# Kernel tuning notes

Measured on AMD Instinct MI355X. Metric: run time of the kernel, lower is better.

The kernel has to match this reference:

```python
import jax, jax.numpy as jnp
import numpy as np

WS = (7, 7)          # window size
N = WS[0] * WS[1]    # 49 tokens per window
C = 128              # dim
H = 4                # num heads
D = C // H           # head dim = 32
B = 8192             # batch * num_windows
NW = 1024            # windows per image
SCALE = D ** -0.5


def _relative_position_index():
    coords_h = np.arange(WS[0])
    coords_w = np.arange(WS[1])
    coords = np.stack(np.meshgrid(coords_h, coords_w, indexing='ij'))  # [2,Wh,Ww]
    flat = coords.reshape(2, -1)                                        # [2,N]
    rel = flat[:, :, None] - flat[:, None, :]                           # [2,N,N]
    rel = rel.transpose(1, 2, 0).astype(np.int64)                       # [N,N,2]
    rel[:, :, 0] += WS[0] - 1
    rel[:, :, 1] += WS[1] - 1
    rel[:, :, 0] *= 2 * WS[1] - 1
    return rel.sum(-1)                                                  # [N,N]


def setup_inputs() -> dict:
    key = jax.random.key(0)
    ks = jax.random.split(key, 8)
    s = 0.02
    return {
        'x': jax.random.normal(ks[0], (B, N, C), jnp.float32),
        'y': jax.random.normal(ks[1], (B, N, C), jnp.float32),
        'mask': jnp.zeros((NW, N, N), jnp.float32),
        'Wq': jax.random.normal(ks[2], (C, C), jnp.float32) * s,
        'bq': jnp.zeros((C,), jnp.float32),
        'Wkv': jax.random.normal(ks[3], (C, 2 * C), jnp.float32) * s,
        'bkv': jnp.zeros((2 * C,), jnp.float32),
        'bias_table': jax.random.normal(ks[4], ((2 * WS[0] - 1) * (2 * WS[1] - 1), H), jnp.float32) * s,
        'Wp': jax.random.normal(ks[5], (C, C), jnp.float32) * s,
        'bp': jnp.zeros((C,), jnp.float32),
        'rel_idx': jnp.asarray(_relative_position_index(), jnp.int32),
    }


def reference(x, y, mask, Wq, bq, Wkv, bkv, bias_table, Wp, bp, rel_idx):
    b = x.shape[0]
    # q/kv projections
    q = (x @ Wq + bq).reshape(b, N, H, D).transpose(0, 2, 1, 3) * SCALE   # [B,H,N,D]
    kv = (y @ Wkv + bkv).reshape(b, N, 2, H, D).transpose(2, 0, 3, 1, 4)  # [2,B,H,N,D]
    k, v = kv[0], kv[1]
    attn = jnp.einsum('bhnd,bhmd->bhnm', q, k)                            # [B,H,N,N]
    # relative position bias gather
    bias = bias_table[rel_idx.reshape(-1)].reshape(N, N, H).transpose(2, 0, 1)  # [H,N,N]
    attn = attn + bias[None]
    # mask add per window
    nW = mask.shape[0]
    attn = attn.reshape(b // nW, nW, H, N, N) + mask[None, :, None]
    attn = attn.reshape(b, H, N, N)
    attn = jax.nn.softmax(attn, axis=-1)
    out = jnp.einsum('bhnm,bhmd->bhnd', attn, v)                          # [B,H,N,D]
    out = out.transpose(0, 2, 1, 3).reshape(b, N, C)
    return out @ Wp + bp
```

## Files before the change

kernel.cpp:

```cpp
#include <hip/hip_runtime.h>
#include <cstddef>


#define MFMA16 __builtin_amdgcn_mfma_f32_16x16x32_bf16

typedef float f32x4 __attribute__((ext_vector_type(4)));
typedef __bf16 bf16x8 __attribute__((ext_vector_type(8)));
typedef __bf16 bf16x4 __attribute__((ext_vector_type(4)));

constexpr int NTOK = 49;
constexpr int CDIM = 128;
constexpr int NWIN = 1024;
constexpr int NB = 8192;
constexpr float SCALE_F = 0.17677669529663687f;

__device__ __forceinline__ int sw128(int row, int col) {
  return (row << 8) + ((((col >> 3) ^ row) & 15) << 4) + ((col & 7) << 1);
}
__device__ __forceinline__ int sw64(int row, int col) {
  return (row << 7) + ((((col >> 3) ^ (row >> 1)) & 7) << 4) + ((col & 7) << 1);
}
__device__ __forceinline__ int swp(int m, int nl) {
  return (m << 6) + ((((nl >> 3) ^ (m >> 1)) & 3) << 4) + ((nl & 7) << 1);
}

__global__ void prepack_kernel(const float* __restrict__ Wq, const float* __restrict__ Wkv,
                               const float* __restrict__ Wp, const float* __restrict__ bias_table,
                               const int* __restrict__ rel_idx,
                               unsigned short* __restrict__ wFrag, float* __restrict__ biasM) {
  int t = blockIdx.x * 256 + threadIdx.x;
  if (t < 8192) {
    const int mat = t >> 11;
    const int g = t & 2047;
    const int frag = g >> 6, lane = g & 63;
    const int nt = frag >> 2, ks = frag & 3;
    const int li = lane & 15, q4 = lane >> 4;
    const int n = nt * 16 + li;
    bf16x8 tmp;
#pragma unroll
    for (int j = 0; j < 8; ++j) {
      const int k = ks * 32 + q4 * 8 + j;
      float v;
      if (mat == 0) v = Wq[k * 128 + n];
      else if (mat == 1) v = Wkv[k * 256 + n];
      else if (mat == 2) v = Wkv[k * 256 + 128 + n];
      else v = Wp[k * 128 + n];
      tmp[j] = (__bf16)v;
    }
    *(bf16x8*)(wFrag + (size_t)t * 8) = tmp;
  } else {
    const int tb = t - 8192;
    if (tb < 4 * 49 * 64) {
      const int h = tb / 3136;
      const int rem = tb - h * 3136;
      const int m = rem >> 6, n = rem & 63;
      float v = 0.f;
      if (n < NTOK) v = bias_table[rel_idx[m * 49 + n] * 4 + h];
      biasM[tb] = v;
    }
  }
}

__global__ void maskM_kernel(const float* __restrict__ mask, float* __restrict__ maskM) {
  __shared__ float sm[2401];
  const int w = blockIdx.x;
  for (int i = threadIdx.x; i < 2401; i += 256) sm[i] = mask[(size_t)w * 2401 + i];
  __syncthreads();
  for (int i = threadIdx.x; i < 3136; i += 256) {
    const int m = i >> 6, n = i & 63;
    maskM[(size_t)w * 3136 + i] = (n < NTOK) ? sm[m * 49 + n] : -1e30f;
  }
}

template <bool PADMASK>
__global__ __launch_bounds__(256, 4) void attn_kernel(
    const float* __restrict__ x, const float* __restrict__ y, const float* __restrict__ maskp,
    const float* __restrict__ bq, const float* __restrict__ bkv, const float* __restrict__ bp,
    const unsigned short* __restrict__ wFrag, const float* __restrict__ biasM,
    float* __restrict__ out) {
  __shared__ __align__(16) unsigned char lds[32768];
  const int tid = threadIdx.x;
  const int w = tid >> 6;
  const int lane = tid & 63;
  const int li = lane & 15;
  const int q4 = lane >> 4;
  const int b = blockIdx.x;
  const int mh = w >> 1;
  const int nh = w & 1;

  bf16x8 ax[2][4], ay[2][4];
#pragma unroll
  for (int t = 0; t < 2; ++t) {
    const int mrow = mh * 32 + t * 16 + li;
    const bool mv = mrow < NTOK;
    const float* xr = x + ((size_t)b * NTOK + (mv ? mrow : 0)) * CDIM;
    const float* yr = y + ((size_t)b * NTOK + (mv ? mrow : 0)) * CDIM;
#pragma unroll
    for (int ks = 0; ks < 4; ++ks) {
      const int c0 = ks * 32 + q4 * 8;
      float4 a0 = *(const float4*)(xr + c0);
      float4 a1 = *(const float4*)(xr + c0 + 4);
      float4 b0 = *(const float4*)(yr + c0);
      float4 b1 = *(const float4*)(yr + c0 + 4);
      if (!mv) {
        a0.x = a0.y = a0.z = a0.w = 0.f; a1.x = a1.y = a1.z = a1.w = 0.f;
        b0.x = b0.y = b0.z = b0.w = 0.f; b1.x = b1.y = b1.z = b1.w = 0.f;
      }
      bf16x8 ta, tb;
      ta[0] = (__bf16)a0.x; ta[1] = (__bf16)a0.y; ta[2] = (__bf16)a0.z; ta[3] = (__bf16)a0.w;
      ta[4] = (__bf16)a1.x; ta[5] = (__bf16)a1.y; ta[6] = (__bf16)a1.z; ta[7] = (__bf16)a1.w;
      tb[0] = (__bf16)b0.x; tb[1] = (__bf16)b0.y; tb[2] = (__bf16)b0.z; tb[3] = (__bf16)b0.w;
      tb[4] = (__bf16)b1.x; tb[5] = (__bf16)b1.y; tb[6] = (__bf16)b1.z; tb[7] = (__bf16)b1.w;
      ax[t][ks] = ta;
      ay[t][ks] = tb;
    }
  }

  const unsigned short* wq = wFrag + 0 * 16384 + nh * 8192;
  const unsigned short* wk = wFrag + 1 * 16384 + nh * 8192;
  const unsigned short* wv = wFrag + 2 * 16384 + nh * 8192;
  const unsigned short* wp = wFrag + 3 * 16384 + nh * 8192;

  auto ldw = [&](const unsigned short* base, int ntl, bf16x8* dst) {
#pragma unroll
    for (int ks = 0; ks < 4; ++ks)
      dst[ks] = *(const bf16x8*)(base + (ntl * 4 + ks) * 512 + lane * 8);
  };

  bf16x8 wfb[2][4];
  bf16x4 vpk[2][4];
  ldw(wq, 0, wfb[0]);
#pragma unroll
  for (int s = 0; s < 12; ++s) {
    if (s < 11) {
      const int nn = s + 1;
      ldw(nn < 4 ? wq : (nn < 8 ? wk : wv), nn & 3, wfb[nn & 1]);
    }
    const int mat = s >> 2, ntl = s & 3;
    const bf16x8* wf = wfb[s & 1];
    if (mat < 2) {
      const int ch0 = nh * 64 + ntl * 16 + q4 * 4;
      const float4 b4 = *(const float4*)((mat == 0 ? bq : bkv) + ch0);
      const int ldsoff = (mat == 0) ? 0 : 16384;
#pragma unroll
      for (int t = 0; t < 2; ++t) {
        const bf16x8* af = (mat == 0) ? &ax[t][0] : &ay[t][0];
        f32x4 acc = {0.f, 0.f, 0.f, 0.f};
#pragma unroll
        for (int ks = 0; ks < 4; ++ks) acc = MFMA16(wf[ks], af[ks], acc, 0, 0, 0);
        const int tok = mh * 32 + t * 16 + li;
        bf16x4 pv;
        pv[0] = (__bf16)(acc[0] + b4.x); pv[1] = (__bf16)(acc[1] + b4.y);
        pv[2] = (__bf16)(acc[2] + b4.z); pv[3] = (__bf16)(acc[3] + b4.w);
        *(bf16x4*)(lds + ldsoff + sw128(tok, ch0)) = pv;
      }
    } else {
      const int nV = nh * 64 + ntl * 16 + li;
      const float bvv = bkv[128 + nV];
#pragma unroll
      for (int t = 0; t < 2; ++t) {
        f32x4 acc = {0.f, 0.f, 0.f, 0.f};
#pragma unroll
        for (int ks = 0; ks < 4; ++ks) acc = MFMA16(ay[t][ks], wf[ks], acc, 0, 0, 0);
        bf16x4 vv4;
        vv4[0] = (__bf16)(acc[0] + bvv); vv4[1] = (__bf16)(acc[1] + bvv);
        vv4[2] = (__bf16)(acc[2] + bvv); vv4[3] = (__bf16)(acc[3] + bvv);
        vpk[t][ntl] = vv4;
      }
    }
  }
  __syncthreads();

  const int h = w;
  unsigned char* const pbase = lds + w * 4096;
  bf16x8 aqf[4], bkf[4];
#pragma unroll
  for (int mt = 0; mt < 4; ++mt)
    aqf[mt] = *(const bf16x8*)(lds + sw128(mt * 16 + li, h * 32 + q4 * 8));
#pragma unroll
  for (int nt = 0; nt < 4; ++nt)
    bkf[nt] = *(const bf16x8*)(lds + 16384 + sw128(nt * 16 + li, h * 32 + q4 * 8));

  const float* __restrict__ biasw = biasM + h * 3136;
  const float* __restrict__ maskw =
      PADMASK ? maskp + (size_t)(b & (NWIN - 1)) * 3136 : maskp + (size_t)(b & (NWIN - 1)) * 2401;

  auto ldbm = [&](int mt, f32x4* dst) {
    const int m = mt * 16 + li;
    const int mm = (m < NTOK ? m : 0);
#pragma unroll
    for (int nt = 0; nt < 4; ++nt) {
      const int nc = nt * 16 + q4 * 4;
      const f32x4 bv = *(const f32x4*)(biasw + mm * 64 + nc);
      f32x4 mv;
      if (PADMASK) {
        mv = *(const f32x4*)(maskw + mm * 64 + nc);
      } else {
#pragma unroll
        for (int r = 0; r < 4; ++r) {
          const int n = nc + r;
          mv[r] = (n < NTOK) ? maskw[mm * 49 + n] : -1e30f;
        }
      }
      dst[nt] = bv + mv;
    }
  };

  f32x4 bmv[2][4];
  ldbm(0, bmv[0]);
  __syncthreads();

#pragma unroll
  for (int ntl = 0; ntl < 4; ++ntl) {
    const int nV = nh * 64 + ntl * 16 + li;
#pragma unroll
    for (int t = 0; t < 2; ++t)
      *(bf16x4*)(lds + 16384 + sw64(nV, mh * 32 + t * 16 + q4 * 4)) = vpk[t][ntl];
  }

  float inv4[4];
  bf16x4 pHi[4][2];
  const f32x4 zz = {0.f, 0.f, 0.f, 0.f};
#pragma unroll
  for (int mt = 0; mt < 4; ++mt) {
    if (mt < 3) ldbm(mt + 1, bmv[(mt + 1) & 1]);
    f32x4 s4[4];
#pragma unroll
    for (int nt = 0; nt < 4; ++nt) s4[nt] = MFMA16(bkf[nt], aqf[mt], zz, 0, 0, 0);
    const f32x4* bm = bmv[mt & 1];
    float vv[4][4];
    float mx = -3.0e38f;
#pragma unroll
    for (int nt = 0; nt < 4; ++nt)
#pragma unroll
      for (int r = 0; r < 4; ++r) {
        const float tv = fmaf(SCALE_F, s4[nt][r], bm[nt][r]);
        vv[nt][r] = tv;
        mx = fmaxf(mx, tv);
      }
    mx = fmaxf(mx, __shfl_xor(mx, 16));
    mx = fmaxf(mx, __shfl_xor(mx, 32));
    float sm = 0.f;
#pragma unroll
    for (int nt = 0; nt < 4; ++nt)
#pragma unroll
      for (int r = 0; r < 4; ++r) {
        const float e = __expf(vv[nt][r] - mx);
        vv[nt][r] = e;
        sm += e;
      }
    sm += __shfl_xor(sm, 16);
    sm += __shfl_xor(sm, 32);
    inv4[mt] = __builtin_amdgcn_rcpf(sm);
    bf16x4 p0, p1;
    p0[0] = (__bf16)vv[0][0]; p0[1] = (__bf16)vv[0][1];
    p0[2] = (__bf16)vv[0][2]; p0[3] = (__bf16)vv[0][3];
    p1[0] = (__bf16)vv[1][0]; p1[1] = (__bf16)vv[1][1];
    p1[2] = (__bf16)vv[1][2]; p1[3] = (__bf16)vv[1][3];
    *(bf16x4*)(pbase + swp(mt * 16 + li, q4 * 4)) = p0;
    *(bf16x4*)(pbase + swp(mt * 16 + li, 16 + q4 * 4)) = p1;
    bf16x4 h0, h1;
    h0[0] = (__bf16)vv[2][0]; h0[1] = (__bf16)vv[2][1];
    h0[2] = (__bf16)vv[2][2]; h0[3] = (__bf16)vv[2][3];
    h1[0] = (__bf16)vv[3][0]; h1[1] = (__bf16)vv[3][1];
    h1[2] = (__bf16)vv[3][2]; h1[3] = (__bf16)vv[3][3];
    pHi[mt][0] = h0;
    pHi[mt][1] = h1;
  }
  __syncthreads();

  bf16x8 bv2[2][2];
#pragma unroll
  for (int cht = 0; cht < 2; ++cht)
#pragma unroll
    for (int ksn = 0; ksn < 2; ++ksn)
      bv2[cht][ksn] =
          *(const bf16x8*)(lds + 16384 + sw64(h * 32 + cht * 16 + li, ksn * 32 + q4 * 8));
  f32x4 o[2][4];
  {
    bf16x8 ap[4];
#pragma unroll
    for (int mt = 0; mt < 4; ++mt)
      ap[mt] = *(const bf16x8*)(pbase + swp(mt * 16 + li, q4 * 8));
#pragma unroll
    for (int cht = 0; cht < 2; ++cht)
#pragma unroll
      for (int mt = 0; mt < 4; ++mt) o[cht][mt] = MFMA16(bv2[cht][0], ap[mt], zz, 0, 0, 0);
#pragma unroll
    for (int mt = 0; mt < 4; ++mt) {
      *(bf16x4*)(pbase + swp(mt * 16 + li, q4 * 4)) = pHi[mt][0];
      *(bf16x4*)(pbase + swp(mt * 16 + li, 16 + q4 * 4)) = pHi[mt][1];
    }
#pragma unroll
    for (int mt = 0; mt < 4; ++mt)
      ap[mt] = *(const bf16x8*)(pbase + swp(mt * 16 + li, q4 * 8));
#pragma unroll
    for (int cht = 0; cht < 2; ++cht)
#pragma unroll
      for (int mt = 0; mt < 4; ++mt)
        o[cht][mt] = MFMA16(bv2[cht][1], ap[mt], o[cht][mt], 0, 0, 0);
  }
  __syncthreads();

#pragma unroll
  for (int cht = 0; cht < 2; ++cht)
#pragma unroll
    for (int mt = 0; mt < 4; ++mt) {
      bf16x4 zv;
      zv[0] = (__bf16)(o[cht][mt][0] * inv4[mt]);
      zv[1] = (__bf16)(o[cht][mt][1] * inv4[mt]);
      zv[2] = (__bf16)(o[cht][mt][2] * inv4[mt]);
      zv[3] = (__bf16)(o[cht][mt][3] * inv4[mt]);
      *(bf16x4*)(lds + sw128(mt * 16 + li, h * 32 + cht * 16 + q4 * 4)) = zv;
    }
  ldw(wp, 0, wfb[0]);
  __syncthreads();

  bf16x8 az[2][4];
#pragma unroll
  for (int t = 0; t < 2; ++t)
#pragma unroll
    for (int ks = 0; ks < 4; ++ks)
      az[t][ks] = *(const bf16x8*)(lds + sw128(mh * 32 + t * 16 + li, ks * 32 + q4 * 8));
#pragma unroll
  for (int ntl = 0; ntl < 4; ++ntl) {
    if (ntl < 3) ldw(wp, ntl + 1, wfb[(ntl + 1) & 1]);
    const bf16x8* wf = wfb[ntl & 1];
    const int ch0 = nh * 64 + ntl * 16 + q4 * 4;
    const float4 b4 = *(const float4*)(bp + ch0);
#pragma unroll
    for (int t = 0; t < 2; ++t) {
      f32x4 acc = {0.f, 0.f, 0.f, 0.f};
#pragma unroll
      for (int ks = 0; ks < 4; ++ks) acc = MFMA16(wf[ks], az[t][ks], acc, 0, 0, 0);
      const int tok = mh * 32 + t * 16 + li;
      if (tok < NTOK) {
        float4 st;
        st.x = acc[0] + b4.x; st.y = acc[1] + b4.y;
        st.z = acc[2] + b4.z; st.w = acc[3] + b4.w;
        *(float4*)(out + ((size_t)b * NTOK + tok) * CDIM + ch0) = st;
      }
    }
  }
}

extern "C" void kernel_launch(void* const* d_in, const int* in_sizes, int n_in, void* d_out,
                              int out_size, void* d_ws, size_t ws_size, hipStream_t stream) {
  const float* x = (const float*)d_in[0];
  const float* y = (const float*)d_in[1];
  const float* mask = (const float*)d_in[2];
  const float* Wq = (const float*)d_in[3];
  const float* bq = (const float*)d_in[4];
  const float* Wkv = (const float*)d_in[5];
  const float* bkv = (const float*)d_in[6];
  const float* bt = (const float*)d_in[7];
  const float* Wp = (const float*)d_in[8];
  const float* bp = (const float*)d_in[9];
  const int* rel = (const int*)d_in[10];
  float* out = (float*)d_out;

  unsigned short* wFrag = (unsigned short*)d_ws;
  float* biasM = (float*)((char*)d_ws + 131072);
  float* maskM = (float*)((char*)d_ws + 181248);
  const size_t needM = 181248 + (size_t)NWIN * 3136 * sizeof(float);

  prepack_kernel<<<96, 256, 0, stream>>>(Wq, Wkv, Wp, bt, rel, wFrag, biasM);
  if (ws_size >= needM) {
    maskM_kernel<<<NWIN, 256, 0, stream>>>(mask, maskM);
    attn_kernel<true><<<NB, 256, 0, stream>>>(x, y, maskM, bq, bkv, bp, wFrag, biasM, out);
  } else {
    attn_kernel<false><<<NB, 256, 0, stream>>>(x, y, mask, bq, bkv, bp, wFrag, biasM, out);
  }
}
```

Measured before the change: 703.0 us.

## Presum bias+mask per window-head, defer V projection, triple-buffer weights, add setprio

Replaces the padded mask table with a per-window, per-head table that already holds relative-position bias plus mask, so the attention loop does one load instead of two loads and an add. This table is four times larger, which adds more preprocessing writes and more L2/HBM traffic. The V projection now runs after the first barrier, overlapping it with the Q/K fragment reads, and weight fragments go through a three-deep register buffer. MFMA blocks are wrapped in s_setprio, launch bounds drop from 4 to 3 blocks per SM, and masking of padded x/y rows is removed, which may raise register use and lower occupancy.

Result: faster. 638.4 us (-9.2%).

```diff
diff --git a/kernel.cpp b/kernel.cpp
--- a/kernel.cpp
+++ b/kernel.cpp
@@ -61,19 +61,33 @@
   }
 }
 
-__global__ void maskM_kernel(const float* __restrict__ mask, float* __restrict__ maskM) {
-  __shared__ float sm[2401];
+__global__ void bmsum_kernel(const float* __restrict__ mask, const float* __restrict__ bias_table,
+                             const int* __restrict__ rel_idx, float* __restrict__ bmSum) {
+  __shared__ float smk[2401];
+  __shared__ int ri[2401];
+  __shared__ float bt[169 * 4];
   const int w = blockIdx.x;
-  for (int i = threadIdx.x; i < 2401; i += 256) sm[i] = mask[(size_t)w * 2401 + i];
+  for (int i = threadIdx.x; i < 2401; i += 256) {
+    smk[i] = mask[(size_t)w * 2401 + i];
+    ri[i] = rel_idx[i];
+  }
+  for (int i = threadIdx.x; i < 676; i += 256) bt[i] = bias_table[i];
   __syncthreads();
   for (int i = threadIdx.x; i < 3136; i += 256) {
     const int m = i >> 6, n = i & 63;
-    maskM[(size_t)w * 3136 + i] = (n < NTOK) ? sm[m * 49 + n] : -1e30f;
-  }
-}
-
-template <bool PADMASK>
-__global__ __launch_bounds__(256, 4) void attn_kernel(
+    const bool valid = (n < NTOK);
+    const int mi = m * 49 + (valid ? n : 0);
+    const float base = smk[mi];
+    const int r = ri[mi];
+#pragma unroll
+    for (int h = 0; h < 4; ++h) {
+      bmSum[((size_t)w * 4 + h) * 3136 + i] = valid ? (bt[r * 4 + h] + base) : -1e30f;
+    }
+  }
+}
+
+template <bool PRESUM>
+__global__ __launch_bounds__(256, 3) void attn_kernel(
     const float* __restrict__ x, const float* __restrict__ y, const float* __restrict__ maskp,
     const float* __restrict__ bq, const float* __restrict__ bkv, const float* __restrict__ bp,
     const unsigned short* __restrict__ wFrag, const float* __restrict__ biasM,
@@ -92,20 +106,16 @@
 #pragma unroll
   for (int t = 0; t < 2; ++t) {
     const int mrow = mh * 32 + t * 16 + li;
-    const bool mv = mrow < NTOK;
-    const float* xr = x + ((size_t)b * NTOK + (mv ? mrow : 0)) * CDIM;
-    const float* yr = y + ((size_t)b * NTOK + (mv ? mrow : 0)) * CDIM;
+    const int mm = mrow < NTOK ? mrow : 0;
+    const float* xr = x + ((size_t)b * NTOK + mm) * CDIM;
+    const float* yr = y + ((size_t)b * NTOK + mm) * CDIM;
 #pragma unroll
     for (int ks = 0; ks < 4; ++ks) {
       const int c0 = ks * 32 + q4 * 8;
-      float4 a0 = *(const float4*)(xr + c0);
-      float4 a1 = *(const float4*)(xr + c0 + 4);
-      float4 b0 = *(const float4*)(yr + c0);
-      float4 b1 = *(const float4*)(yr + c0 + 4);
-      if (!mv) {
-        a0.x = a0.y = a0.z = a0.w = 0.f; a1.x = a1.y = a1.z = a1.w = 0.f;
-        b0.x = b0.y = b0.z = b0.w = 0.f; b1.x = b1.y = b1.z = b1.w = 0.f;
-      }
+      const float4 a0 = *(const float4*)(xr + c0);
+      const float4 a1 = *(const float4*)(xr + c0 + 4);
+      const float4 b0 = *(const float4*)(yr + c0);
+      const float4 b1 = *(const float4*)(yr + c0 + 4);
       bf16x8 ta, tb;
       ta[0] = (__bf16)a0.x; ta[1] = (__bf16)a0.y; ta[2] = (__bf16)a0.z; ta[3] = (__bf16)a0.w;
       ta[4] = (__bf16)a1.x; ta[5] = (__bf16)a1.y; ta[6] = (__bf16)a1.z; ta[7] = (__bf16)a1.w;
@@ -120,6 +130,7 @@
   const unsigned short* wk = wFrag + 1 * 16384 + nh * 8192;
   const unsigned short* wv = wFrag + 2 * 16384 + nh * 8192;
   const unsigned short* wp = wFrag + 3 * 16384 + nh * 8192;
+  const unsigned short* mats01[2] = {wq, wk};
 
   auto ldw = [&](const unsigned short* base, int ntl, bf16x8* dst) {
 #pragma unroll
@@ -127,48 +138,35 @@
       dst[ks] = *(const bf16x8*)(base + (ntl * 4 + ks) * 512 + lane * 8);
   };
 
-  bf16x8 wfb[2][4];
-  bf16x4 vpk[2][4];
+  bf16x8 wfb[3][4];
   ldw(wq, 0, wfb[0]);
-#pragma unroll
-  for (int s = 0; s < 12; ++s) {
-    if (s < 11) {
-      const int nn = s + 1;
-      ldw(nn < 4 ? wq : (nn < 8 ? wk : wv), nn & 3, wfb[nn & 1]);
+  ldw(wq, 1, wfb[1]);
+#pragma unroll
+  for (int s = 0; s < 8; ++s) {
+    if (s < 6) {
+      const int nn = s + 2;
+      ldw(mats01[nn >> 2], nn & 3, wfb[nn % 3]);
     }
     const int mat = s >> 2, ntl = s & 3;
-    const bf16x8* wf = wfb[s & 1];
-    if (mat < 2) {
-      const int ch0 = nh * 64 + ntl * 16 + q4 * 4;
-      const float4 b4 = *(const float4*)((mat == 0 ? bq : bkv) + ch0);
-      const int ldsoff = (mat == 0) ? 0 : 16384;
-#pragma unroll
-      for (int t = 0; t < 2; ++t) {
-        const bf16x8* af = (mat == 0) ? &ax[t][0] : &ay[t][0];
-        f32x4 acc = {0.f, 0.f, 0.f, 0.f};
-#pragma unroll
-        for (int ks = 0; ks < 4; ++ks) acc = MFMA16(wf[ks], af[ks], acc, 0, 0, 0);
-        const int tok = mh * 32 + t * 16 + li;
-        bf16x4 pv;
-        pv[0] = (__bf16)(acc[0] + b4.x); pv[1] = (__bf16)(acc[1] + b4.y);
-        pv[2] = (__bf16)(acc[2] + b4.z); pv[3] = (__bf16)(acc[3] + b4.w);
-        *(bf16x4*)(lds + ldsoff + sw128(tok, ch0)) = pv;
-      }
-    } else {
-      const int nV = nh * 64 + ntl * 16 + li;
-      const float bvv = bkv[128 + nV];
-#pragma unroll
-      for (int t = 0; t < 2; ++t) {
-        f32x4 acc = {0.f, 0.f, 0.f, 0.f};
-#pragma unroll
-        for (int ks = 0; ks < 4; ++ks) acc = MFMA16(ay[t][ks], wf[ks], acc, 0, 0, 0);
-        bf16x4 vv4;
-        vv4[0] = (__bf16)(acc[0] + bvv); vv4[1] = (__bf16)(acc[1] + bvv);
-        vv4[2] = (__bf16)(acc[2] + bvv); vv4[3] = (__bf16)(acc[3] + bvv);
-        vpk[t][ntl] = vv4;
-      }
-    }
-  }
+    const bf16x8* wf = wfb[s % 3];
+    const int ch0 = nh * 64 + ntl * 16 + q4 * 4;
+    const float4 b4 = *(const float4*)((mat == 0 ? bq : bkv) + ch0);
+    const int ldsoff = (mat == 0) ? 0 : 16384;
+#pragma unroll
+    for (int t = 0; t < 2; ++t) {
+      const bf16x8* af = (mat == 0) ? &ax[t][0] : &ay[t][0];
+      f32x4 acc = {0.f, 0.f, 0.f, 0.f};
+#pragma unroll
+      for (int ks = 0; ks < 4; ++ks) acc = MFMA16(wf[ks], af[ks], acc, 0, 0, 0);
+      const int tok = mh * 32 + t * 16 + li;
+      bf16x4 pv;
+      pv[0] = (__bf16)(acc[0] + b4.x); pv[1] = (__bf16)(acc[1] + b4.y);
+      pv[2] = (__bf16)(acc[2] + b4.z); pv[3] = (__bf16)(acc[3] + b4.w);
+      *(bf16x4*)(lds + ldsoff + sw128(tok, ch0)) = pv;
+    }
+  }
+  ldw(wv, 0, wfb[0]);
+  ldw(wv, 1, wfb[1]);
   __syncthreads();
 
   const int h = w;
@@ -181,9 +179,30 @@
   for (int nt = 0; nt < 4; ++nt)
     bkf[nt] = *(const bf16x8*)(lds + 16384 + sw128(nt * 16 + li, h * 32 + q4 * 8));
 
+  bf16x4 vpk[2][4];
+#pragma unroll
+  for (int v = 0; v < 4; ++v) {
+    if (v < 2) ldw(wv, v + 2, wfb[(v + 2) % 3]);
+    const bf16x8* wf = wfb[v % 3];
+    const int nV = nh * 64 + v * 16 + li;
+    const float bvv = bkv[128 + nV];
+#pragma unroll
+    for (int t = 0; t < 2; ++t) {
+      f32x4 acc = {0.f, 0.f, 0.f, 0.f};
+#pragma unroll
+      for (int ks = 0; ks < 4; ++ks) acc = MFMA16(ay[t][ks], wf[ks], acc, 0, 0, 0);
+      bf16x4 vv4;
+      vv4[0] = (__bf16)(acc[0] + bvv); vv4[1] = (__bf16)(acc[1] + bvv);
+      vv4[2] = (__bf16)(acc[2] + bvv); vv4[3] = (__bf16)(acc[3] + bvv);
+      vpk[t][v] = vv4;
+    }
+  }
+
+  const float* __restrict__ bmw =
+      PRESUM ? maskp + ((size_t)(b & (NWIN - 1)) * 4 + h) * 3136 : nullptr;
   const float* __restrict__ biasw = biasM + h * 3136;
   const float* __restrict__ maskw =
-      PADMASK ? maskp + (size_t)(b & (NWIN - 1)) * 3136 : maskp + (size_t)(b & (NWIN - 1)) * 2401;
+      PRESUM ? nullptr : maskp + (size_t)(b & (NWIN - 1)) * 2401;
 
   auto ldbm = [&](int mt, f32x4* dst) {
     const int m = mt * 16 + li;
@@ -191,18 +210,18 @@
 #pragma unroll
     for (int nt = 0; nt < 4; ++nt) {
       const int nc = nt * 16 + q4 * 4;
-      const f32x4 bv = *(const f32x4*)(biasw + mm * 64 + nc);
-      f32x4 mv;
-      if (PADMASK) {
-        mv = *(const f32x4*)(maskw + mm * 64 + nc);
+      if (PRESUM) {
+        dst[nt] = *(const f32x4*)(bmw + mm * 64 + nc);
       } else {
+        const f32x4 bv = *(const f32x4*)(biasw + mm * 64 + nc);
+        f32x4 mv;
 #pragma unroll
         for (int r = 0; r < 4; ++r) {
           const int n = nc + r;
           mv[r] = (n < NTOK) ? maskw[mm * 49 + n] : -1e30f;
         }
+        dst[nt] = bv + mv;
       }
-      dst[nt] = bv + mv;
     }
   };
 
@@ -225,8 +244,10 @@
   for (int mt = 0; mt < 4; ++mt) {
     if (mt < 3) ldbm(mt + 1, bmv[(mt + 1) & 1]);
     f32x4 s4[4];
+    __builtin_amdgcn_s_setprio(1);
 #pragma unroll
     for (int nt = 0; nt < 4; ++nt) s4[nt] = MFMA16(bkf[nt], aqf[mt], zz, 0, 0, 0);
+    __builtin_amdgcn_s_setprio(0);
     const f32x4* bm = bmv[mt & 1];
     float vv[4][4];
     float mx = -3.0e38f;
@@ -282,10 +303,12 @@
 #pragma unroll
     for (int mt = 0; mt < 4; ++mt)
       ap[mt] = *(const bf16x8*)(pbase + swp(mt * 16 + li, q4 * 8));
+    __builtin_amdgcn_s_setprio(1);
 #pragma unroll
     for (int cht = 0; cht < 2; ++cht)
 #pragma unroll
       for (int mt = 0; mt < 4; ++mt) o[cht][mt] = MFMA16(bv2[cht][0], ap[mt], zz, 0, 0, 0);
+    __builtin_amdgcn_s_setprio(0);
 #pragma unroll
     for (int mt = 0; mt < 4; ++mt) {
       *(bf16x4*)(pbase + swp(mt * 16 + li, q4 * 4)) = pHi[mt][0];
@@ -294,11 +317,13 @@
 #pragma unroll
     for (int mt = 0; mt < 4; ++mt)
       ap[mt] = *(const bf16x8*)(pbase + swp(mt * 16 + li, q4 * 8));
+    __builtin_amdgcn_s_setprio(1);
 #pragma unroll
     for (int cht = 0; cht < 2; ++cht)
 #pragma unroll
       for (int mt = 0; mt < 4; ++mt)
         o[cht][mt] = MFMA16(bv2[cht][1], ap[mt], o[cht][mt], 0, 0, 0);
+    __builtin_amdgcn_s_setprio(0);
   }
   __syncthreads();
 
@@ -314,6 +339,7 @@
       *(bf16x4*)(lds + sw128(mt * 16 + li, h * 32 + cht * 16 + q4 * 4)) = zv;
     }
   ldw(wp, 0, wfb[0]);
+  ldw(wp, 1, wfb[1]);
   __syncthreads();
 
   bf16x8 az[2][4];
@@ -324,8 +350,8 @@
       az[t][ks] = *(const bf16x8*)(lds + sw128(mh * 32 + t * 16 + li, ks * 32 + q4 * 8));
 #pragma unroll
   for (int ntl = 0; ntl < 4; ++ntl) {
-    if (ntl < 3) ldw(wp, ntl + 1, wfb[(ntl + 1) & 1]);
-    const bf16x8* wf = wfb[ntl & 1];
+    if (ntl < 2) ldw(wp, ntl + 2, wfb[(ntl + 2) % 3]);
+    const bf16x8* wf = wfb[ntl % 3];
     const int ch0 = nh * 64 + ntl * 16 + q4 * 4;
     const float4 b4 = *(const float4*)(bp + ch0);
 #pragma unroll
@@ -361,13 +387,13 @@
 
   unsigned short* wFrag = (unsigned short*)d_ws;
   float* biasM = (float*)((char*)d_ws + 131072);
-  float* maskM = (float*)((char*)d_ws + 181248);
-  const size_t needM = 181248 + (size_t)NWIN * 3136 * sizeof(float);
+  float* bmSum = (float*)((char*)d_ws + 181248);
+  const size_t needS = 181248 + (size_t)NWIN * 4 * 3136 * sizeof(float);
 
   prepack_kernel<<<96, 256, 0, stream>>>(Wq, Wkv, Wp, bt, rel, wFrag, biasM);
-  if (ws_size >= needM) {
-    maskM_kernel<<<NWIN, 256, 0, stream>>>(mask, maskM);
-    attn_kernel<true><<<NB, 256, 0, stream>>>(x, y, maskM, bq, bkv, bp, wFrag, biasM, out);
+  if (ws_size >= needS) {
+    bmsum_kernel<<<NWIN, 256, 0, stream>>>(mask, bt, rel, bmSum);
+    attn_kernel<true><<<NB, 256, 0, stream>>>(x, y, bmSum, bq, bkv, bp, wFrag, biasM, out);
   } else {
     attn_kernel<false><<<NB, 256, 0, stream>>>(x, y, mask, bq, bkv, bp, wFrag, biasM, out);
   }
```
